# Optimization experiments

Measured on AMD Instinct MI355X. Metric: run time of the kernel, lower is better.

The kernel has to match this reference:

```python
import jax, jax.numpy as jnp
import numpy as np

GATE_INIT_BIAS = -0.6931471805599453  # -log(2)

def mish(x):
    return x * jnp.tanh(jax.nn.softplus(x))

def setup_inputs() -> dict:
    key = jax.random.key(0)
    ks = jax.random.split(key, 24)
    B = 262144
    x = jax.random.normal(ks[0], (B, 18), dtype=jnp.float32)
    band = jax.random.randint(ks[1], (B,), 0, 9).astype(jnp.float32)
    x = x.at[:, 17].set(band)
    def lin(k, fan_in, shape):
        bound = 1.0 / np.sqrt(fan_in)
        return jax.random.uniform(k, shape, jnp.float32, -bound, bound)
    inp = {
        'x': x,
        # trunk: 15->512->256 (Mish)
        'tw1': lin(ks[2], 15, (15, 512)),  'tb1': lin(ks[3], 15, (512,)),
        'tw2': lin(ks[4], 512, (512, 256)), 'tb2': lin(ks[5], 512, (256,)),
        # 9 band heads: 256->128->1, stacked on leading axis
        'hw1': lin(ks[6], 256, (9, 256, 128)), 'hb1': lin(ks[7], 256, (9, 128)),
        'hw2': lin(ks[8], 128, (9, 128)),      'hb2': lin(ks[9], 128, (9,)),
        # sun scaler head 256->64->1 (final layer zero weight, bias = gate_init_bias)
        'sw1': lin(ks[10], 256, (256, 64)), 'sb1': lin(ks[11], 256, (64,)),
        'sw2': jnp.zeros((64, 1), jnp.float32), 'sb2': jnp.full((1,), GATE_INIT_BIAS, jnp.float32),
        # storm scaler head
        'stw1': lin(ks[12], 256, (256, 64)), 'stb1': lin(ks[13], 256, (64,)),
        'stw2': jnp.zeros((64, 1), jnp.float32), 'stb2': jnp.full((1,), GATE_INIT_BIAS, jnp.float32),
        # monotonic sidecars: 1->8->1, softplus-positivized weights
        'sun_w1': lin(ks[14], 1, (1, 8)),  'sun_b1': lin(ks[15], 1, (8,)),
        'sun_w2': lin(ks[16], 8, (8, 1)),  'sun_b2': lin(ks[17], 8, (1,)),
        'storm_w1': lin(ks[18], 1, (1, 8)), 'storm_b1': lin(ks[19], 1, (8,)),
        'storm_w2': lin(ks[20], 8, (8, 1)), 'storm_b2': lin(ks[21], 8, (1,)),
    }
    return inp

def monotonic_mlp(v, w1, b1, w2, b2):
    # MonotonicMLP: positivity via softplus on weights, tanh hidden activation
    h = jnp.tanh(v @ jax.nn.softplus(w1) + b1)
    return h @ jax.nn.softplus(w2) + b2  # [B,1]

def reference(x, tw1, tb1, tw2, tb2, hw1, hb1, hw2, hb2,
              sw1, sb1, sw2, sb2, stw1, stb1, stw2, stb2,
              sun_w1, sun_b1, sun_w2, sun_b2,
              storm_w1, storm_b1, storm_w2, storm_b2):
    x_deep = x[:, :15]
    x_sfi = x[:, 15:16]
    x_kp = x[:, 16:17]
    band = x[:, 17].astype(jnp.int32)  # [B]

    # trunk
    t = mish(mish(x_deep @ tw1 + tb1) @ tw2 + tb2)  # [B,256]

    # all 9 band heads densely (faithful to original), then gather
    hh = mish(jnp.einsum('bd,kdh->bkh', t, hw1) + hb1)       # [B,9,128]
    all_heads = jnp.einsum('bkh,kh->bk', hh, hw2) + hb2      # [B,9]
    base_snr = jnp.take_along_axis(all_heads, band[:, None], axis=1)  # [B,1]

    sun_logit = mish(t @ sw1 + sb1) @ sw2 + sb2      # [B,1]
    storm_logit = mish(t @ stw1 + stb1) @ stw2 + stb2
    sun_gate = jax.nn.sigmoid(sun_logit)
    storm_gate = jax.nn.sigmoid(storm_logit)

    return base_snr + sun_gate * monotonic_mlp(x_sfi, sun_w1, sun_b1, sun_w2, sun_b2) \
                    + storm_gate * monotonic_mlp(x_kp, storm_w1, storm_b1, storm_w2, storm_b2)
```

## Files before the change

### kernel.cpp

```cpp
#include <hip/hip_runtime.h>
#include <cstdint>

typedef unsigned short u16;
typedef unsigned char u8;
typedef __attribute__((ext_vector_type(8))) __bf16 bf16x8;
typedef __attribute__((ext_vector_type(4))) float f32x4;

#define MFMA16(a, b, c) __builtin_amdgcn_mfma_f32_16x16x32_bf16((a), (b), (c), 0, 0, 0)

__device__ __forceinline__ u16 f2b(float f) {
    union { float f; unsigned u; } v; v.f = f;
    unsigned r = v.u + 0x7fffu + ((v.u >> 16) & 1u);
    return (u16)(r >> 16);
}
__device__ __forceinline__ u16 f2b_hw(float f) {
    union { __bf16 h; u16 u; } cv; cv.h = (__bf16)f; return cv.u;
}
__device__ __forceinline__ float b2f(u16 h) {
    union { unsigned u; float f; } v; v.u = ((unsigned)h) << 16; return v.f;
}
__device__ __forceinline__ float fast_rcp(float x) { return __builtin_amdgcn_rcpf(x); }
__device__ __forceinline__ float mish_f(float x) {
    float s = __expf(fminf(x, 40.0f));
    float p = s * (s + 2.0f);
    return x * p * fast_rcp(p + 2.0f);
}
__device__ __forceinline__ float tanh_f(float y) {
    float e = __expf(2.0f * y);
    return 1.0f - 2.0f * fast_rcp(e + 1.0f);
}
__device__ __forceinline__ float sigmoid_f(float y) {
    return fast_rcp(1.0f + __expf(-y));
}
__device__ __forceinline__ float splus(float w) { return log1pf(__expf(w)); }

template <int CTRL>
__device__ __forceinline__ float dpp_add(float v) {
    union { float f; int i; } s, p;
    s.f = v;
    p.i = __builtin_amdgcn_update_dpp(0, s.i, CTRL, 0xf, 0xf, true);
    return v + p.f;
}
__device__ __forceinline__ float row16_sum(float v) {
    v = dpp_add<0xB1>(v);
    v = dpp_add<0x4E>(v);
    v = dpp_add<0x141>(v);
    v = dpp_add<0x140>(v);
    return v;
}

#define WS_PERM      0u
#define WS_GOFF      1048576u
#define WS_BBAND     1048640u
#define WS_BSTART    1065088u
#define WS_BNROWS    1081536u
#define WS_SP        1097984u
#define WS_GPART     1098112u
#define WS_CPRE      1116544u
#define WS_BANDS     1134976u
#define WS_W1P       1397120u
#define WS_W2F       1429888u
#define WS_HW1F      1692032u
#define WS_SWF       2281856u
#define WS_STWF      2314624u
#define WS_NEEDED    2347392u

#define PACK_BLOCKS  512


__global__ void k_pack(const float* __restrict__ x, int B,
                       const float* __restrict__ tw1, const float* __restrict__ tw2,
                       const float* __restrict__ hw1,
                       const float* __restrict__ sw1, const float* __restrict__ stw1,
                       const float* __restrict__ sun_w1, const float* __restrict__ sun_w2,
                       const float* __restrict__ storm_w1, const float* __restrict__ storm_w2,
                       u16* __restrict__ W1p, u16* __restrict__ W2f, u16* __restrict__ HWf,
                       u16* __restrict__ SWf, u16* __restrict__ STWf,
                       float* __restrict__ sp, int* __restrict__ gpart,
                       u8* __restrict__ bands)
{
    __shared__ int h[9];
    int ltid = threadIdx.x;
    int tid = blockIdx.x * blockDim.x + ltid;
    if (ltid < 9) h[ltid] = 0;
    __syncthreads();
    const int CH = B / PACK_BLOCKS;
    const int base = blockIdx.x * CH;
    for (int i = ltid; i < CH; i += 256) {
        int r = base + i;
        int b = (int)x[r * 18 + 17];
        bands[r] = (u8)b;
        atomicAdd(&h[b], 1);
    }

    if (tid < 32) {
        const float* srcs[4] = { sun_w1, sun_w2, storm_w1, storm_w2 };
        float w = srcs[tid >> 3][tid & 7];
        sp[tid] = splus(w);
    }
    const int total = 16384 + 131072 + 294912 + 16384 + 16384;
    for (int i = tid; i < total; i += PACK_BLOCKS * 256) {
        int idx = i;
        if (idx < 16384) {
            int n = idx >> 5, k = idx & 31;
            W1p[idx] = (k < 15) ? f2b(tw1[k * 512 + n]) : (u16)0;
        } else if ((idx -= 16384) < 131072) {
            int tile = idx >> 9, within = idx & 511;
            int lane = within >> 3, j = within & 7;
            int nt = tile >> 4, kb = tile & 15;
            int n = nt * 16 + (lane & 15);
            int k = kb * 32 + (lane >> 4) * 8 + j;
            W2f[idx] = f2b(tw2[k * 256 + n]);
        } else if ((idx -= 131072) < 294912) {
            int g = idx >> 15, r = idx & 32767;
            int tile = r >> 9, within = r & 511;
            int lane = within >> 3, j = within & 7;
            int nt = tile >> 3, kb = tile & 7;
            int n = nt * 16 + (lane & 15);
            int k = kb * 32 + (lane >> 4) * 8 + j;
            HWf[idx] = f2b(hw1[(g * 256 + k) * 128 + n]);
        } else if ((idx -= 294912) < 16384) {
            int tile = idx >> 9, within = idx & 511;
            int lane = within >> 3, j = within & 7;
            int nt = tile >> 3, kb = tile & 7;
            int n = nt * 16 + (lane & 15);
            int k = kb * 32 + (lane >> 4) * 8 + j;
            SWf[idx] = f2b(sw1[k * 64 + n]);
        } else {
            idx -= 16384;
            int tile = idx >> 9, within = idx & 511;
            int lane = within >> 3, j = within & 7;
            int nt = tile >> 3, kb = tile & 7;
            int n = nt * 16 + (lane & 15);
            int k = kb * 32 + (lane >> 4) * 8 + j;
            STWf[idx] = f2b(stw1[k * 64 + n]);
        }
    }
    __syncthreads();
    if (ltid < 9) gpart[blockIdx.x * 9 + ltid] = h[ltid];
}

__global__ void k_table(const int* __restrict__ gpart, int* __restrict__ cpre,
                        int* __restrict__ blk_band,
                        int* __restrict__ blk_start, int* __restrict__ blk_nrows, int nblk_max)
{
    __shared__ int s_goff[10], s_bstart[10], s_cnt[9];
    int tid = threadIdx.x;
    if (tid < 9) {
        int s = 0;
        for (int c = 0; c < PACK_BLOCKS; ++c) s += gpart[c * 9 + tid];
        s_cnt[tid] = s;
    }
    __syncthreads();
    if (tid == 0) {
        int off = 0, boff = 0;
        for (int g = 0; g < 9; ++g) {
            s_goff[g] = off;
            s_bstart[g] = boff;
            off += s_cnt[g];
            boff += (s_cnt[g] + 63) >> 6;
        }
        s_goff[9] = off;
        s_bstart[9] = boff;
    }
    __syncthreads();
    if (tid < 9) {
        int run = s_goff[tid];
        for (int c = 0; c < PACK_BLOCKS; ++c) {
            cpre[c * 9 + tid] = run;
            run += gpart[c * 9 + tid];
        }
    }
    for (int b = tid; b < nblk_max; b += blockDim.x) {
        int band = -1, loc = 0;
        for (int g = 0; g < 9; ++g)
            if (b >= s_bstart[g] && b < s_bstart[g + 1]) { band = g; loc = b - s_bstart[g]; }
        blk_band[b] = band;
        if (band >= 0) {
            blk_start[b] = s_goff[band] + loc * 64;
            int rem = s_cnt[band] - loc * 64;
            blk_nrows[b] = rem < 64 ? rem : 64;
        } else { blk_start[b] = 0; blk_nrows[b] = 0; }
    }
}

__global__ __launch_bounds__(512) void k_scatter(const u8* __restrict__ bands,
                                                 const int* __restrict__ cpre,
                                                 int* __restrict__ perm, int B)
{
    __shared__ int wcnt[8][9];
    __shared__ int wpre[8][9];
    int tid = threadIdx.x;
    int lane = tid & 63, wave = tid >> 6;
    int i = blockIdx.x * 512 + tid;
    int band = -1, rank = 0;
    if (i < B) band = (int)bands[i];
    for (int k = 0; k < 9; ++k) {
        unsigned long long m = __ballot(band == k);
        if (band == k) rank = __popcll(m & ((1ull << lane) - 1ull));
        if (lane == 0) wcnt[wave][k] = __popcll(m);
    }
    __syncthreads();
    if (tid < 9) {
        int run = 0;
        for (int w = 0; w < 8; ++w) { wpre[w][tid] = run; run += wcnt[w][tid]; }
    }
    __syncthreads();
    if (i < B && band >= 0)
        perm[cpre[blockIdx.x * 9 + band] + wpre[wave][band] + rank] = i;
}

__global__ __launch_bounds__(512, 4) void k_main(
                       const float* __restrict__ x,
                       const int* __restrict__ perm,
                       const int* __restrict__ blk_band,
                       const int* __restrict__ blk_start,
                       const int* __restrict__ blk_nrows,
                       const u16* __restrict__ W1p, const u16* __restrict__ W2f,
                       const u16* __restrict__ HWf,
                       const u16* __restrict__ SWf, const u16* __restrict__ STWf,
                       const float* __restrict__ tb1, const float* __restrict__ tb2,
                       const float* __restrict__ hb1, const float* __restrict__ hw2,
                       const float* __restrict__ hb2,
                       const float* __restrict__ sb1, const float* __restrict__ sw2,
                       const float* __restrict__ sb2,
                       const float* __restrict__ stb1, const float* __restrict__ stw2,
                       const float* __restrict__ stb2,
                       const float* __restrict__ sp,
                       const float* __restrict__ sun_b1, const float* __restrict__ sun_b2,
                       const float* __restrict__ storm_b1, const float* __restrict__ storm_b2,
                       float* __restrict__ out)
{
    int bb = blk_band[blockIdx.x];
    if (bb < 0) return;
    int rstart = blk_start[blockIdx.x];
    int nrows  = blk_nrows[blockIdx.x];

    __shared__ union {
        u16 xA[64][32];
        float red[16][64];
    } su;
    __shared__ int rowsL[64];
    __shared__ float sfiL[64], kpL[64];
    __shared__ u16 buf[2][64][136];

    int tid = threadIdx.x;
    int lane = tid & 63, wave = tid >> 6;
    int quad = lane >> 4, l15 = lane & 15;

    if (tid < 64) {
        int r = rstart + (tid < nrows ? tid : 0);
        rowsL[tid] = perm[r];
    }
    for (int i = tid; i < 64 * 32; i += 512) ((u16*)su.xA)[i] = 0;
    __syncthreads();
    for (int i = tid; i < 64 * 18; i += 512) {
        int r = i / 18, c = i - r * 18;
        float v = x[rowsL[r] * 18 + c];
        if (c < 15) su.xA[r][c] = f2b_hw(v);
        else if (c == 15) sfiL[r] = v;
        else if (c == 16) kpL[r] = v;
    }
    __syncthreads();

    bf16x8 ax[4];
#pragma unroll
    for (int mt = 0; mt < 4; ++mt)
        ax[mt] = *(const bf16x8*)&su.xA[mt * 16 + l15][quad * 8];

    f32x4 acc2[2][4] = {};

    for (int c = 0; c < 4; ++c) {
        f32x4 acc1[4] = {};
        {
            int ncol = c * 128 + wave * 16 + l15;
            bf16x8 bw = *(const bf16x8*)&W1p[ncol * 32 + quad * 8];
#pragma unroll
            for (int mt = 0; mt < 4; ++mt)
                acc1[mt] = MFMA16(ax[mt], bw, acc1[mt]);
        }
        u16 (*bufc)[136] = buf[c & 1];
        {
            int ccol = wave * 16 + l15;
            float bias = tb1[c * 128 + ccol];
#pragma unroll
            for (int mt = 0; mt < 4; ++mt)
#pragma unroll
                for (int r = 0; r < 4; ++r)
                    bufc[mt * 16 + quad * 4 + r][ccol] = f2b_hw(mish_f(acc1[mt][r] + bias));
        }
        __syncthreads();
        for (int ks = 0; ks < 4; ++ks) {
            bf16x8 a2[4];
#pragma unroll
            for (int mt = 0; mt < 4; ++mt)
                a2[mt] = *(const bf16x8*)&bufc[mt * 16 + l15][ks * 32 + quad * 8];
            int kb = c * 4 + ks;
#pragma unroll
            for (int ntl = 0; ntl < 2; ++ntl) {
                int nt = wave * 2 + ntl;
                bf16x8 bw = *(const bf16x8*)&W2f[((nt * 16 + kb) << 9) + lane * 8];
#pragma unroll
                for (int mt = 0; mt < 4; ++mt)
                    acc2[ntl][mt] = MFMA16(a2[mt], bw, acc2[ntl][mt]);
            }
        }
    }
    __syncthreads();

    u16 (*tmat)[264] = (u16(*)[264])buf;
#pragma unroll
    for (int ntl = 0; ntl < 2; ++ntl) {
        int col = wave * 32 + ntl * 16 + l15;
        float bias = tb2[col];
#pragma unroll
        for (int mt = 0; mt < 4; ++mt)
#pragma unroll
            for (int r = 0; r < 4; ++r)
                tmat[mt * 16 + quad * 4 + r][col] = f2b_hw(mish_f(acc2[ntl][mt][r] + bias));
    }
    __syncthreads();

    f32x4 acch[4] = {}, accg[4] = {};
    const u16* Hw = HWf + bb * 32768;
    const u16* Gw = (wave < 4) ? SWf : STWf;
    int gnt = wave & 3;
    for (int kb = 0; kb < 8; ++kb) {
        bf16x8 a3[4];
#pragma unroll
        for (int mt = 0; mt < 4; ++mt)
            a3[mt] = *(const bf16x8*)&tmat[mt * 16 + l15][kb * 32 + quad * 8];
        bf16x8 bh = *(const bf16x8*)&Hw[((wave * 8 + kb) << 9) + lane * 8];
        bf16x8 bg = *(const bf16x8*)&Gw[((gnt * 8 + kb) << 9) + lane * 8];
#pragma unroll
        for (int mt = 0; mt < 4; ++mt) {
            acch[mt] = MFMA16(a3[mt], bh, acch[mt]);
            accg[mt] = MFMA16(a3[mt], bg, accg[mt]);
        }
    }

    float hsum[4][4];
    {
        int col = wave * 16 + l15;
        float hb = hb1[bb * 128 + col];
        float wv = hw2[bb * 128 + col];
#pragma unroll
        for (int mt = 0; mt < 4; ++mt)
#pragma unroll
            for (int r = 0; r < 4; ++r)
                hsum[mt][r] = mish_f(acch[mt][r] + hb) * wv;
    }
    float gsum[4][4];
    {
        int n = gnt * 16 + l15;
        float gb = (wave < 4) ? sb1[n] : stb1[n];
        float gw = (wave < 4) ? sw2[n] : stw2[n];
#pragma unroll
        for (int mt = 0; mt < 4; ++mt)
#pragma unroll
            for (int r = 0; r < 4; ++r)
                gsum[mt][r] = mish_f(accg[mt][r] + gb) * gw;
    }
#pragma unroll
    for (int mt = 0; mt < 4; ++mt)
#pragma unroll
        for (int r = 0; r < 4; ++r) {
            hsum[mt][r] = row16_sum(hsum[mt][r]);
            gsum[mt][r] = row16_sum(gsum[mt][r]);
        }
    if (l15 == 0)
#pragma unroll
        for (int mt = 0; mt < 4; ++mt)
#pragma unroll
            for (int r = 0; r < 4; ++r) {
                int row = mt * 16 + quad * 4 + r;
                su.red[wave][row] = hsum[mt][r];
                su.red[8 + wave][row] = gsum[mt][r];
            }
    __syncthreads();

    if (tid < 64 && tid < nrows) {
        int row = tid;
        float head = hb2[bb];
#pragma unroll
        for (int w = 0; w < 8; ++w) head += su.red[w][row];
        float sl = sb2[0], tl = stb2[0];
#pragma unroll
        for (int w = 0; w < 4; ++w) { sl += su.red[8 + w][row]; tl += su.red[12 + w][row]; }
        float sg = sigmoid_f(sl);
        float tg = sigmoid_f(tl);
        float v1 = sfiL[row], v2 = kpL[row];
        float sun_val = sun_b2[0], storm_val = storm_b2[0];
#pragma unroll
        for (int j = 0; j < 8; ++j) {
            sun_val   += tanh_f(v1 * sp[j]      + sun_b1[j])   * sp[8 + j];
            storm_val += tanh_f(v2 * sp[16 + j] + storm_b1[j]) * sp[24 + j];
        }
        out[rowsL[row]] = head + sg * sun_val + tg * storm_val;
    }
}

__global__ __launch_bounds__(64) void k_simple(
    const float* __restrict__ x,
    const float* __restrict__ tw1, const float* __restrict__ tb1,
    const float* __restrict__ tw2, const float* __restrict__ tb2,
    const float* __restrict__ hw1, const float* __restrict__ hb1,
    const float* __restrict__ hw2, const float* __restrict__ hb2,
    const float* __restrict__ sw1, const float* __restrict__ sb1,
    const float* __restrict__ sw2, const float* __restrict__ sb2,
    const float* __restrict__ stw1, const float* __restrict__ stb1,
    const float* __restrict__ stw2, const float* __restrict__ stb2,
    const float* __restrict__ sun_w1, const float* __restrict__ sun_b1,
    const float* __restrict__ sun_w2, const float* __restrict__ sun_b2,
    const float* __restrict__ storm_w1, const float* __restrict__ storm_b1,
    const float* __restrict__ storm_w2, const float* __restrict__ storm_b2,
    float* __restrict__ out)
{
    __shared__ u16 t_lds[256 * 64];

    const int lane = threadIdx.x;
    const int r = blockIdx.x * 64 + lane;

    float xr[15];
#pragma unroll
    for (int k = 0; k < 15; ++k) xr[k] = x[r * 18 + k];
    const float sfi = x[r * 18 + 15];
    const float kp  = x[r * 18 + 16];
    const int band  = (int)x[r * 18 + 17];

    for (int tc = 0; tc < 4; ++tc) {
        float acc[64];
#pragma unroll
        for (int j = 0; j < 64; ++j) acc[j] = 0.0f;
        for (int n = 0; n < 512; ++n) {
            float p = tb1[n];
#pragma unroll
            for (int k = 0; k < 15; ++k) p += xr[k] * tw1[k * 512 + n];
            const float a1n = mish_f(p);
            const float* w2 = &tw2[n * 256 + tc * 64];
#pragma unroll
            for (int j = 0; j < 64; ++j) acc[j] += a1n * w2[j];
        }
#pragma unroll
        for (int j = 0; j < 64; ++j)
            t_lds[(tc * 64 + j) * 64 + lane] = f2b(mish_f(acc[j] + tb2[tc * 64 + j]));
    }
    __syncthreads();

    float head_val = 0.0f;
    for (int g = 0; g < 9; ++g) {
        float hs = 0.0f;
        for (int hc = 0; hc < 2; ++hc) {
            float pre[64];
#pragma unroll
            for (int j = 0; j < 64; ++j) pre[j] = 0.0f;
            for (int d = 0; d < 256; ++d) {
                const float td = b2f(t_lds[d * 64 + lane]);
                const float* wv = &hw1[g * 32768 + d * 128 + hc * 64];
#pragma unroll
                for (int j = 0; j < 64; ++j) pre[j] += td * wv[j];
            }
#pragma unroll
            for (int j = 0; j < 64; ++j) {
                const int h = hc * 64 + j;
                hs += mish_f(pre[j] + hb1[g * 128 + h]) * hw2[g * 128 + h];
            }
        }
        head_val += (band == g) ? (hs + hb2[g]) : 0.0f;
    }

    float pre_s[64], pre_t[64];
#pragma unroll
    for (int j = 0; j < 64; ++j) { pre_s[j] = 0.0f; pre_t[j] = 0.0f; }
    for (int d = 0; d < 256; ++d) {
        const float td = b2f(t_lds[d * 64 + lane]);
        const float* ws1 = &sw1[d * 64];
        const float* wt1 = &stw1[d * 64];
#pragma unroll
        for (int j = 0; j < 64; ++j) {
            pre_s[j] += td * ws1[j];
            pre_t[j] += td * wt1[j];
        }
    }
    float ls = sb2[0], lt = stb2[0];
#pragma unroll
    for (int j = 0; j < 64; ++j) {
        ls += mish_f(pre_s[j] + sb1[j]) * sw2[j];
        lt += mish_f(pre_t[j] + stb1[j]) * stw2[j];
    }
    const float sg = sigmoid_f(ls);
    const float tg = sigmoid_f(lt);

    float sun_val = sun_b2[0], storm_val = storm_b2[0];
#pragma unroll
    for (int j = 0; j < 8; ++j) {
        sun_val   += tanh_f(sfi * splus(sun_w1[j])  + sun_b1[j])   * splus(sun_w2[j]);
        storm_val += tanh_f(kp * splus(storm_w1[j]) + storm_b1[j]) * splus(storm_w2[j]);
    }

    out[r] = head_val + sg * sun_val + tg * storm_val;
}

extern "C" void kernel_launch(void* const* d_in, const int* in_sizes, int n_in,
                              void* d_out, int out_size, void* d_ws, size_t ws_size,
                              hipStream_t stream) {
    (void)n_in; (void)out_size;
    const float* x        = (const float*)d_in[0];
    const float* tw1      = (const float*)d_in[1];
    const float* tb1      = (const float*)d_in[2];
    const float* tw2      = (const float*)d_in[3];
    const float* tb2      = (const float*)d_in[4];
    const float* hw1      = (const float*)d_in[5];
    const float* hb1      = (const float*)d_in[6];
    const float* hw2      = (const float*)d_in[7];
    const float* hb2      = (const float*)d_in[8];
    const float* sw1      = (const float*)d_in[9];
    const float* sb1      = (const float*)d_in[10];
    const float* sw2      = (const float*)d_in[11];
    const float* sb2      = (const float*)d_in[12];
    const float* stw1     = (const float*)d_in[13];
    const float* stb1     = (const float*)d_in[14];
    const float* stw2     = (const float*)d_in[15];
    const float* stb2     = (const float*)d_in[16];
    const float* sun_w1   = (const float*)d_in[17];
    const float* sun_b1   = (const float*)d_in[18];
    const float* sun_w2   = (const float*)d_in[19];
    const float* sun_b2   = (const float*)d_in[20];
    const float* storm_w1 = (const float*)d_in[21];
    const float* storm_b1 = (const float*)d_in[22];
    const float* storm_w2 = (const float*)d_in[23];
    const float* storm_b2 = (const float*)d_in[24];

    const int B = in_sizes[0] / 18;

    if (ws_size < (size_t)WS_NEEDED) {
        k_simple<<<B / 64, 64, 0, stream>>>(x, tw1, tb1, tw2, tb2, hw1, hb1, hw2, hb2,
                                            sw1, sb1, sw2, sb2, stw1, stb1, stw2, stb2,
                                            sun_w1, sun_b1, sun_w2, sun_b2,
                                            storm_w1, storm_b1, storm_w2, storm_b2,
                                            (float*)d_out);
        return;
    }

    char* ws = (char*)d_ws;
    int*   perm      = (int*)(ws + WS_PERM);
    int*   blk_band  = (int*)(ws + WS_BBAND);
    int*   blk_start = (int*)(ws + WS_BSTART);
    int*   blk_nrows = (int*)(ws + WS_BNROWS);
    float* sp        = (float*)(ws + WS_SP);
    int*   gpart     = (int*)(ws + WS_GPART);
    int*   cpre      = (int*)(ws + WS_CPRE);
    u8*    bands     = (u8*)(ws + WS_BANDS);
    u16*   W1p       = (u16*)(ws + WS_W1P);
    u16*   W2f       = (u16*)(ws + WS_W2F);
    u16*   HWf       = (u16*)(ws + WS_HW1F);
    u16*   SWf       = (u16*)(ws + WS_SWF);
    u16*   STWf      = (u16*)(ws + WS_STWF);

    int nblk = B / 64 + 16;

    k_pack<<<PACK_BLOCKS, 256, 0, stream>>>(x, B, tw1, tw2, hw1, sw1, stw1,
                                            sun_w1, sun_w2, storm_w1, storm_w2,
                                            W1p, W2f, HWf, SWf, STWf, sp, gpart, bands);
    k_table<<<1, 256, 0, stream>>>(gpart, cpre, blk_band, blk_start, blk_nrows, nblk);
    k_scatter<<<PACK_BLOCKS, 512, 0, stream>>>(bands, cpre, perm, B);
    k_main<<<nblk, 512, 0, stream>>>(x, perm, blk_band, blk_start, blk_nrows,
                                     W1p, W2f, HWf, SWf, STWf,
                                     tb1, tb2, hb1, hw2, hb2,
                                     sb1, sw2, sb2, stb1, stw2, stb2,
                                     sp, sun_b1, sun_b2, storm_b1, storm_b2,
                                     (float*)d_out);
}
```

Baseline: 326.6 us.

## Fuse band histogram, table and scatter into one atomic-bucketing pack kernel

```diff
diff --git a/kernel.cpp b/kernel.cpp
--- a/kernel.cpp
+++ b/kernel.cpp
@@ -50,25 +50,20 @@
 }
 
 #define WS_PERM      0u
-#define WS_GOFF      1048576u
-#define WS_BBAND     1048640u
-#define WS_BSTART    1065088u
-#define WS_BNROWS    1081536u
-#define WS_SP        1097984u
-#define WS_GPART     1098112u
-#define WS_CPRE      1116544u
-#define WS_BANDS     1134976u
-#define WS_W1P       1397120u
-#define WS_W2F       1429888u
-#define WS_HW1F      1692032u
-#define WS_SWF       2281856u
-#define WS_STWF      2314624u
-#define WS_NEEDED    2347392u
-
-#define PACK_BLOCKS  512
-
-
-__global__ void k_pack(const float* __restrict__ x, int B,
+#define WS_CNT       1179648u
+#define WS_SP        1183744u
+#define WS_W1P       1184768u
+#define WS_W2F       1217536u
+#define WS_HW1F      1479680u
+#define WS_SWF       2069504u
+#define WS_STWF      2102272u
+#define WS_NEEDED    2135040u
+
+#define CAPH 16384
+#define REG_BLOCKS 256
+
+
+__global__ __launch_bounds__(512) void k_pack(const float* __restrict__ x, int B,
                        const float* __restrict__ tw1, const float* __restrict__ tw2,
                        const float* __restrict__ hw1,
                        const float* __restrict__ sw1, const float* __restrict__ stw1,
@@ -76,146 +71,84 @@
                        const float* __restrict__ storm_w1, const float* __restrict__ storm_w2,
                        u16* __restrict__ W1p, u16* __restrict__ W2f, u16* __restrict__ HWf,
                        u16* __restrict__ SWf, u16* __restrict__ STWf,
-                       float* __restrict__ sp, int* __restrict__ gpart,
-                       u8* __restrict__ bands)
+                       float* __restrict__ sp, int* __restrict__ cnt,
+                       int* __restrict__ perm)
 {
-    __shared__ int h[9];
-    int ltid = threadIdx.x;
-    int tid = blockIdx.x * blockDim.x + ltid;
-    if (ltid < 9) h[ltid] = 0;
-    __syncthreads();
-    const int CH = B / PACK_BLOCKS;
-    const int base = blockIdx.x * CH;
-    for (int i = ltid; i < CH; i += 256) {
-        int r = base + i;
-        int b = (int)x[r * 18 + 17];
-        bands[r] = (u8)b;
-        atomicAdd(&h[b], 1);
-    }
-
-    if (tid < 32) {
+    __shared__ int wcnt[8][9];
+    __shared__ int wpre[8][9];
+    __shared__ int bbase[9];
+    const int tid  = threadIdx.x;
+    const int lane = tid & 63, wave = tid >> 6;
+    const int sub  = blockIdx.x & 1;
+    const int i    = blockIdx.x * 512 + tid;
+
+    int band = -1, rank = 0;
+    if (i < B) band = (int)x[i * 18 + 17];
+    for (int k = 0; k < 9; ++k) {
+        unsigned long long m = __ballot(band == k);
+        if (band == k) rank = __popcll(m & ((1ull << lane) - 1ull));
+        if (lane == 0) wcnt[wave][k] = __popcll(m);
+    }
+    __syncthreads();
+    if (tid < 9) {
+        int run = 0;
+        for (int w = 0; w < 8; ++w) { wpre[w][tid] = run; run += wcnt[w][tid]; }
+        bbase[tid] = atomicAdd(&cnt[(tid * 2 + sub) * 32], run);
+    }
+    __syncthreads();
+    if (band >= 0)
+        perm[(band * 2 + sub) * CAPH + bbase[band] + wpre[wave][band] + rank] = i;
+
+    const int gtid = blockIdx.x * 512 + tid;
+    if (gtid < 32) {
         const float* srcs[4] = { sun_w1, sun_w2, storm_w1, storm_w2 };
-        float w = srcs[tid >> 3][tid & 7];
-        sp[tid] = splus(w);
+        float w = srcs[gtid >> 3][gtid & 7];
+        sp[gtid] = splus(w);
     }
     const int total = 16384 + 131072 + 294912 + 16384 + 16384;
-    for (int i = tid; i < total; i += PACK_BLOCKS * 256) {
-        int idx = i;
+    for (int i2 = gtid; i2 < total; i2 += 512 * 512) {
+        int idx = i2;
         if (idx < 16384) {
             int n = idx >> 5, k = idx & 31;
             W1p[idx] = (k < 15) ? f2b(tw1[k * 512 + n]) : (u16)0;
         } else if ((idx -= 16384) < 131072) {
             int tile = idx >> 9, within = idx & 511;
-            int lane = within >> 3, j = within & 7;
+            int lane2 = within >> 3, j = within & 7;
             int nt = tile >> 4, kb = tile & 15;
-            int n = nt * 16 + (lane & 15);
-            int k = kb * 32 + (lane >> 4) * 8 + j;
+            int n = nt * 16 + (lane2 & 15);
+            int k = kb * 32 + (lane2 >> 4) * 8 + j;
             W2f[idx] = f2b(tw2[k * 256 + n]);
         } else if ((idx -= 131072) < 294912) {
             int g = idx >> 15, r = idx & 32767;
             int tile = r >> 9, within = r & 511;
-            int lane = within >> 3, j = within & 7;
+            int lane2 = within >> 3, j = within & 7;
             int nt = tile >> 3, kb = tile & 7;
-            int n = nt * 16 + (lane & 15);
-            int k = kb * 32 + (lane >> 4) * 8 + j;
+            int n = nt * 16 + (lane2 & 15);
+            int k = kb * 32 + (lane2 >> 4) * 8 + j;
             HWf[idx] = f2b(hw1[(g * 256 + k) * 128 + n]);
         } else if ((idx -= 294912) < 16384) {
             int tile = idx >> 9, within = idx & 511;
-            int lane = within >> 3, j = within & 7;
+            int lane2 = within >> 3, j = within & 7;
             int nt = tile >> 3, kb = tile & 7;
-            int n = nt * 16 + (lane & 15);
-            int k = kb * 32 + (lane >> 4) * 8 + j;
+            int n = nt * 16 + (lane2 & 15);
+            int k = kb * 32 + (lane2 >> 4) * 8 + j;
             SWf[idx] = f2b(sw1[k * 64 + n]);
         } else {
             idx -= 16384;
             int tile = idx >> 9, within = idx & 511;
-            int lane = within >> 3, j = within & 7;
+            int lane2 = within >> 3, j = within & 7;
             int nt = tile >> 3, kb = tile & 7;
-            int n = nt * 16 + (lane & 15);
-            int k = kb * 32 + (lane >> 4) * 8 + j;
+            int n = nt * 16 + (lane2 & 15);
+            int k = kb * 32 + (lane2 >> 4) * 8 + j;
             STWf[idx] = f2b(stw1[k * 64 + n]);
         }
     }
-    __syncthreads();
-    if (ltid < 9) gpart[blockIdx.x * 9 + ltid] = h[ltid];
-}
-
-__global__ void k_table(const int* __restrict__ gpart, int* __restrict__ cpre,
-                        int* __restrict__ blk_band,
-                        int* __restrict__ blk_start, int* __restrict__ blk_nrows, int nblk_max)
-{
-    __shared__ int s_goff[10], s_bstart[10], s_cnt[9];
-    int tid = threadIdx.x;
-    if (tid < 9) {
-        int s = 0;
-        for (int c = 0; c < PACK_BLOCKS; ++c) s += gpart[c * 9 + tid];
-        s_cnt[tid] = s;
-    }
-    __syncthreads();
-    if (tid == 0) {
-        int off = 0, boff = 0;
-        for (int g = 0; g < 9; ++g) {
-            s_goff[g] = off;
-            s_bstart[g] = boff;
-            off += s_cnt[g];
-            boff += (s_cnt[g] + 63) >> 6;
-        }
-        s_goff[9] = off;
-        s_bstart[9] = boff;
-    }
-    __syncthreads();
-    if (tid < 9) {
-        int run = s_goff[tid];
-        for (int c = 0; c < PACK_BLOCKS; ++c) {
-            cpre[c * 9 + tid] = run;
-            run += gpart[c * 9 + tid];
-        }
-    }
-    for (int b = tid; b < nblk_max; b += blockDim.x) {
-        int band = -1, loc = 0;
-        for (int g = 0; g < 9; ++g)
-            if (b >= s_bstart[g] && b < s_bstart[g + 1]) { band = g; loc = b - s_bstart[g]; }
-        blk_band[b] = band;
-        if (band >= 0) {
-            blk_start[b] = s_goff[band] + loc * 64;
-            int rem = s_cnt[band] - loc * 64;
-            blk_nrows[b] = rem < 64 ? rem : 64;
-        } else { blk_start[b] = 0; blk_nrows[b] = 0; }
-    }
-}
-
-__global__ __launch_bounds__(512) void k_scatter(const u8* __restrict__ bands,
-                                                 const int* __restrict__ cpre,
-                                                 int* __restrict__ perm, int B)
-{
-    __shared__ int wcnt[8][9];
-    __shared__ int wpre[8][9];
-    int tid = threadIdx.x;
-    int lane = tid & 63, wave = tid >> 6;
-    int i = blockIdx.x * 512 + tid;
-    int band = -1, rank = 0;
-    if (i < B) band = (int)bands[i];
-    for (int k = 0; k < 9; ++k) {
-        unsigned long long m = __ballot(band == k);
-        if (band == k) rank = __popcll(m & ((1ull << lane) - 1ull));
-        if (lane == 0) wcnt[wave][k] = __popcll(m);
-    }
-    __syncthreads();
-    if (tid < 9) {
-        int run = 0;
-        for (int w = 0; w < 8; ++w) { wpre[w][tid] = run; run += wcnt[w][tid]; }
-    }
-    __syncthreads();
-    if (i < B && band >= 0)
-        perm[cpre[blockIdx.x * 9 + band] + wpre[wave][band] + rank] = i;
 }
 
 __global__ __launch_bounds__(512, 4) void k_main(
                        const float* __restrict__ x,
                        const int* __restrict__ perm,
-                       const int* __restrict__ blk_band,
-                       const int* __restrict__ blk_start,
-                       const int* __restrict__ blk_nrows,
+                       const int* __restrict__ cnt,
                        const u16* __restrict__ W1p, const u16* __restrict__ W2f,
                        const u16* __restrict__ HWf,
                        const u16* __restrict__ SWf, const u16* __restrict__ STWf,
@@ -231,10 +164,13 @@
                        const float* __restrict__ storm_b1, const float* __restrict__ storm_b2,
                        float* __restrict__ out)
 {
-    int bb = blk_band[blockIdx.x];
-    if (bb < 0) return;
-    int rstart = blk_start[blockIdx.x];
-    int nrows  = blk_nrows[blockIdx.x];
+    const int region = blockIdx.x >> 8;
+    const int loc    = blockIdx.x & 255;
+    const int bb     = region >> 1;
+    const int nr0    = cnt[region * 32] - loc * 64;
+    if (nr0 <= 0) return;
+    const int nrows  = nr0 > 64 ? 64 : nr0;
+    const int rstart = region * CAPH + loc * 64;
 
     __shared__ union {
         u16 xA[64][32];
@@ -544,30 +480,22 @@
 
     char* ws = (char*)d_ws;
     int*   perm      = (int*)(ws + WS_PERM);
-    int*   blk_band  = (int*)(ws + WS_BBAND);
-    int*   blk_start = (int*)(ws + WS_BSTART);
-    int*   blk_nrows = (int*)(ws + WS_BNROWS);
+    int*   cnt       = (int*)(ws + WS_CNT);
     float* sp        = (float*)(ws + WS_SP);
-    int*   gpart     = (int*)(ws + WS_GPART);
-    int*   cpre      = (int*)(ws + WS_CPRE);
-    u8*    bands     = (u8*)(ws + WS_BANDS);
     u16*   W1p       = (u16*)(ws + WS_W1P);
     u16*   W2f       = (u16*)(ws + WS_W2F);
     u16*   HWf       = (u16*)(ws + WS_HW1F);
     u16*   SWf       = (u16*)(ws + WS_SWF);
-    u16*   STWf      = (u16*)(ws + WS_STWF);
-
-    int nblk = B / 64 + 16;
-
-    k_pack<<<PACK_BLOCKS, 256, 0, stream>>>(x, B, tw1, tw2, hw1, sw1, stw1,
-                                            sun_w1, sun_w2, storm_w1, storm_w2,
-                                            W1p, W2f, HWf, SWf, STWf, sp, gpart, bands);
-    k_table<<<1, 256, 0, stream>>>(gpart, cpre, blk_band, blk_start, blk_nrows, nblk);
-    k_scatter<<<PACK_BLOCKS, 512, 0, stream>>>(bands, cpre, perm, B);
-    k_main<<<nblk, 512, 0, stream>>>(x, perm, blk_band, blk_start, blk_nrows,
-                                     W1p, W2f, HWf, SWf, STWf,
-                                     tb1, tb2, hb1, hw2, hb2,
-                                     sb1, sw2, sb2, stb1, stw2, stb2,
-                                     sp, sun_b1, sun_b2, storm_b1, storm_b2,
-                                     (float*)d_out);
-}
+    u16*   STWf     = (u16*)(ws + WS_STWF);
+
+    hipMemsetAsync(cnt, 0, 18 * 32 * sizeof(int), stream);
+    k_pack<<<(B + 511) / 512, 512, 0, stream>>>(x, B, tw1, tw2, hw1, sw1, stw1,
+                                                sun_w1, sun_w2, storm_w1, storm_w2,
+                                                W1p, W2f, HWf, SWf, STWf, sp, cnt, perm);
+    k_main<<<18 * REG_BLOCKS, 512, 0, stream>>>(x, perm, cnt,
+                                                W1p, W2f, HWf, SWf, STWf,
+                                                tb1, tb2, hb1, hw2, hb2,
+                                                sb1, sw2, sb2, stb1, stw2, stb2,
+                                                sp, sun_b1, sun_b2, storm_b1, storm_b2,
+                                                (float*)d_out);
+}
```

Result: faster. 304.5 us (-6.8%).
